# Optimization experiments

Hardware: AMD Instinct MI355X
Metric: run time of the kernel (lower is better)

## Reference

```python
import jax, jax.numpy as jnp
import numpy as np

LN_EPS = 1e-5  # torch LayerNorm default


def setup_inputs() -> dict:
    key = jax.random.key(0)
    ks = jax.random.split(key, 8)
    R, B, E, H, NREL = 100, 32, 15000, 16, 237
    return {
        "all_h": jax.random.randint(ks[0], (B,), 0, E, dtype=jnp.int64),
        "all_r": jnp.zeros((B,), dtype=jnp.int64),  # all queries share one relation (asserted in torch code)
        "rule_count": jax.random.randint(ks[1], (R, B, E), 0, 2, dtype=jnp.int32),  # grounding counts (sparse 0/1)
        "rule_emb": jax.random.normal(ks[2], (R, H), dtype=jnp.float32),
        "relation_emb": jax.random.normal(ks[3], (NREL, H), dtype=jnp.float32),
        "ln_g": jnp.ones((H,), dtype=jnp.float32),
        "ln_b": jnp.zeros((H,), dtype=jnp.float32),
        "W1": jax.random.normal(ks[4], (2 * H, 128), dtype=jnp.float32) * 0.1,
        "b1": jnp.zeros((128,), dtype=jnp.float32),
        "W2": jax.random.normal(ks[5], (128, 1), dtype=jnp.float32) * 0.1,
        "b2": jnp.zeros((1,), dtype=jnp.float32),
        "bias": jnp.zeros((E,), dtype=jnp.float32),
    }


def reference(all_h, all_r, rule_count, rule_emb, relation_emb, ln_g, ln_b, W1, b1, W2, b2, bias):
    # rule_count: [R, B, E] grounding counts; candidates are positions with any nonzero count.
    rc = rule_count.astype(jnp.float32)
    cand = rc.sum(0) > 0  # [B, E] candidate mask

    # FuncToNodeSum: weighted sum of rule embeddings per (batch, entity), then LayerNorm + ReLU.
    wvf = jnp.einsum('rbe,rh->beh', rc, rule_emb)  # [B, E, H]
    mu = wvf.mean(-1, keepdims=True)
    var = ((wvf - mu) ** 2).mean(-1, keepdims=True)
    vv = jax.nn.relu((wvf - mu) * jax.lax.rsqrt(var + LN_EPS) * ln_g + ln_b)

    # Concatenate query-relation embedding and score with MLP(2H -> 128 -> 1).
    rel = relation_emb[all_r[0]]  # [H]
    feat = jnp.concatenate([vv, jnp.broadcast_to(rel, vv.shape)], axis=-1)  # [B, E, 2H]
    h = jax.nn.relu(jnp.einsum('beh,hk->bek', feat, W1) + b1)
    out = (jnp.einsum('bek,ko->beo', h, W2) + b2)[..., 0]  # [B, E]

    # Scatter to candidates only (zeros elsewhere), then add entity bias (entity_feature='bias').
    score = jnp.where(cand, out, 0.0) + bias[None, :]
    return score
```

## Files before the change

kernel.cpp:

```cpp
#include <hip/hip_runtime.h>

#define NRULE 100
#define NB    32
#define NE    15000
#define NTOT  (NB * NE)
#define HD    16
#define KMID  128
#define LN_EPS 1e-5f

__global__ void precompute_c_kernel(const int* __restrict__ all_r,
                                    const float* __restrict__ relemb,
                                    const float* __restrict__ W1,
                                    const float* __restrict__ b1,
                                    float* __restrict__ cvec)
{
    const int k = threadIdx.x;
    if (k >= KMID) return;
    const int r = all_r[0];
    float t = b1[k];
#pragma unroll
    for (int h = 0; h < HD; ++h)
        t = fmaf(relemb[r * HD + h], W1[(HD + h) * KMID + k], t);
    cvec[k] = t;
}

__global__ __launch_bounds__(256) void predictor_main_kernel(
    const int*   __restrict__ rc,
    const float* __restrict__ remb,
    const float* __restrict__ ln_g,
    const float* __restrict__ ln_b,
    const float* __restrict__ W1,
    const float* __restrict__ W2,
    const float* __restrict__ b2,
    const float* __restrict__ bias,
    const float* __restrict__ cvec,
    float* __restrict__ out)
{
    const int tid  = blockIdx.x * blockDim.x + threadIdx.x;
    const int base = tid * 2;
    if (base >= NTOT) return;

    float acc0[HD], acc1[HD];
#pragma unroll
    for (int h = 0; h < HD; ++h) { acc0[h] = 0.f; acc1[h] = 0.f; }
    float ws0 = 0.f, ws1 = 0.f;

    const int* rcp = rc + base;
#pragma unroll 4
    for (int r = 0; r < NRULE; ++r) {
        const int2 p = *reinterpret_cast<const int2*>(rcp + r * NTOT);
        const float v0 = (float)p.x;
        const float v1 = (float)p.y;
        ws0 += v0; ws1 += v1;
#pragma unroll
        for (int h = 0; h < HD; ++h) {
            const float w = remb[r * HD + h];
            acc0[h] = fmaf(v0, w, acc0[h]);
            acc1[h] = fmaf(v1, w, acc1[h]);
        }
    }

    float vv0[HD], vv1[HD];
    {
        float mu0 = 0.f, mu1 = 0.f;
#pragma unroll
        for (int h = 0; h < HD; ++h) { mu0 += acc0[h]; mu1 += acc1[h]; }
        mu0 *= (1.f / HD); mu1 *= (1.f / HD);
        float var0 = 0.f, var1 = 0.f;
#pragma unroll
        for (int h = 0; h < HD; ++h) {
            const float d0 = acc0[h] - mu0;
            const float d1 = acc1[h] - mu1;
            var0 = fmaf(d0, d0, var0);
            var1 = fmaf(d1, d1, var1);
        }
        var0 *= (1.f / HD); var1 *= (1.f / HD);
        const float ri0 = rsqrtf(var0 + LN_EPS);
        const float ri1 = rsqrtf(var1 + LN_EPS);
#pragma unroll
        for (int h = 0; h < HD; ++h) {
            const float g = ln_g[h], bb = ln_b[h];
            vv0[h] = fmaxf(fmaf((acc0[h] - mu0) * ri0, g, bb), 0.f);
            vv1[h] = fmaxf(fmaf((acc1[h] - mu1) * ri1, g, bb), 0.f);
        }
    }

    const float b2v = b2[0];
    float o0 = b2v, o1 = b2v;
#pragma unroll 1
    for (int kc = 0; kc < KMID; kc += 16) {
        float t0[16], t1[16];
#pragma unroll
        for (int kk = 0; kk < 16; ++kk) {
            const float c = cvec[kc + kk];
            t0[kk] = c; t1[kk] = c;
        }
#pragma unroll
        for (int h = 0; h < HD; ++h) {
            const float a0 = vv0[h], a1 = vv1[h];
#pragma unroll
            for (int kk = 0; kk < 16; ++kk) {
                const float w = W1[h * KMID + kc + kk];
                t0[kk] = fmaf(a0, w, t0[kk]);
                t1[kk] = fmaf(a1, w, t1[kk]);
            }
        }
#pragma unroll
        for (int kk = 0; kk < 16; ++kk) {
            const float w2 = W2[kc + kk];
            o0 = fmaf(fmaxf(t0[kk], 0.f), w2, o0);
            o1 = fmaf(fmaxf(t1[kk], 0.f), w2, o1);
        }
    }

    o0 = (ws0 > 0.f) ? o0 : 0.f;
    o1 = (ws1 > 0.f) ? o1 : 0.f;
    const int m = base % NE;
    float2 res;
    res.x = o0 + bias[m];
    res.y = o1 + bias[m + 1];
    *reinterpret_cast<float2*>(out + base) = res;
}

extern "C" void kernel_launch(void* const* d_in, const int* in_sizes, int n_in,
                              void* d_out, int out_size, void* d_ws, size_t ws_size,
                              hipStream_t stream)
{
    const int*   all_r  = (const int*)d_in[1];
    const int*   rc     = (const int*)d_in[2];
    const float* remb   = (const float*)d_in[3];
    const float* relemb = (const float*)d_in[4];
    const float* ln_g   = (const float*)d_in[5];
    const float* ln_b   = (const float*)d_in[6];
    const float* W1     = (const float*)d_in[7];
    const float* b1     = (const float*)d_in[8];
    const float* W2     = (const float*)d_in[9];
    const float* b2     = (const float*)d_in[10];
    const float* bias   = (const float*)d_in[11];
    float* out  = (float*)d_out;
    float* cvec = (float*)d_ws;

    hipLaunchKernelGGL(precompute_c_kernel, dim3(1), dim3(128), 0, stream,
                       all_r, relemb, W1, b1, cvec);

    const int threads = NTOT / 2;
    const int blocks  = (threads + 255) / 256;
    hipLaunchKernelGGL(predictor_main_kernel, dim3(blocks), dim3(256), 0, stream,
                       rc, remb, ln_g, ln_b, W1, W2, b2, bias, cvec, out);
}
```

Before: 71.97 us.

## Use one element per thread with batched rule-count loads and higher occupancy

```diff
diff --git a/kernel.cpp b/kernel.cpp
--- a/kernel.cpp
+++ b/kernel.cpp
@@ -7,6 +7,7 @@
 #define HD    16
 #define KMID  128
 #define LN_EPS 1e-5f
+#define RCHUNK 20
 
 __global__ void precompute_c_kernel(const int* __restrict__ all_r,
                                     const float* __restrict__ relemb,
@@ -24,7 +25,7 @@
     cvec[k] = t;
 }
 
-__global__ __launch_bounds__(256) void predictor_main_kernel(
+__global__ __launch_bounds__(256, 8) void predictor_main_kernel(
     const int*   __restrict__ rc,
     const float* __restrict__ remb,
     const float* __restrict__ ln_g,
@@ -36,90 +37,69 @@
     const float* __restrict__ cvec,
     float* __restrict__ out)
 {
-    const int tid  = blockIdx.x * blockDim.x + threadIdx.x;
-    const int base = tid * 2;
-    if (base >= NTOT) return;
+    const int tid = blockIdx.x * blockDim.x + threadIdx.x;
+    if (tid >= NTOT) return;
 
-    float acc0[HD], acc1[HD];
+    float acc[HD];
 #pragma unroll
-    for (int h = 0; h < HD; ++h) { acc0[h] = 0.f; acc1[h] = 0.f; }
-    float ws0 = 0.f, ws1 = 0.f;
+    for (int h = 0; h < HD; ++h) acc[h] = 0.f;
+    float ws = 0.f;
 
-    const int* rcp = rc + base;
-#pragma unroll 4
-    for (int r = 0; r < NRULE; ++r) {
-        const int2 p = *reinterpret_cast<const int2*>(rcp + r * NTOT);
-        const float v0 = (float)p.x;
-        const float v1 = (float)p.y;
-        ws0 += v0; ws1 += v1;
+    const int* rcp = rc + tid;
 #pragma unroll
-        for (int h = 0; h < HD; ++h) {
-            const float w = remb[r * HD + h];
-            acc0[h] = fmaf(v0, w, acc0[h]);
-            acc1[h] = fmaf(v1, w, acc1[h]);
+    for (int r0 = 0; r0 < NRULE; r0 += RCHUNK) {
+        int v[RCHUNK];
+#pragma unroll
+        for (int i = 0; i < RCHUNK; ++i)
+            v[i] = rcp[(r0 + i) * NTOT];
+#pragma unroll
+        for (int i = 0; i < RCHUNK; ++i) {
+            const float f = (float)v[i];
+            ws += f;
+#pragma unroll
+            for (int h = 0; h < HD; ++h)
+                acc[h] = fmaf(f, remb[(r0 + i) * HD + h], acc[h]);
         }
     }
 
-    float vv0[HD], vv1[HD];
     {
-        float mu0 = 0.f, mu1 = 0.f;
+        float mu = 0.f;
 #pragma unroll
-        for (int h = 0; h < HD; ++h) { mu0 += acc0[h]; mu1 += acc1[h]; }
-        mu0 *= (1.f / HD); mu1 *= (1.f / HD);
-        float var0 = 0.f, var1 = 0.f;
+        for (int h = 0; h < HD; ++h) mu += acc[h];
+        mu *= (1.f / HD);
+        float var = 0.f;
 #pragma unroll
         for (int h = 0; h < HD; ++h) {
-            const float d0 = acc0[h] - mu0;
-            const float d1 = acc1[h] - mu1;
-            var0 = fmaf(d0, d0, var0);
-            var1 = fmaf(d1, d1, var1);
+            const float d = acc[h] - mu;
+            var = fmaf(d, d, var);
         }
-        var0 *= (1.f / HD); var1 *= (1.f / HD);
-        const float ri0 = rsqrtf(var0 + LN_EPS);
-        const float ri1 = rsqrtf(var1 + LN_EPS);
+        var *= (1.f / HD);
+        const float ri = rsqrtf(var + LN_EPS);
+#pragma unroll
+        for (int h = 0; h < HD; ++h)
+            acc[h] = fmaxf(fmaf((acc[h] - mu) * ri, ln_g[h], ln_b[h]), 0.f);
+    }
+
+    float o = b2[0];
+#pragma unroll 1
+    for (int kc = 0; kc < KMID; kc += 16) {
+        float t[16];
+#pragma unroll
+        for (int kk = 0; kk < 16; ++kk) t[kk] = cvec[kc + kk];
 #pragma unroll
         for (int h = 0; h < HD; ++h) {
-            const float g = ln_g[h], bb = ln_b[h];
-            vv0[h] = fmaxf(fmaf((acc0[h] - mu0) * ri0, g, bb), 0.f);
-            vv1[h] = fmaxf(fmaf((acc1[h] - mu1) * ri1, g, bb), 0.f);
+            const float a = acc[h];
+#pragma unroll
+            for (int kk = 0; kk < 16; ++kk)
+                t[kk] = fmaf(a, W1[h * KMID + kc + kk], t[kk]);
         }
+#pragma unroll
+        for (int kk = 0; kk < 16; ++kk)
+            o = fmaf(fmaxf(t[kk], 0.f), W2[kc + kk], o);
     }
 
-    const float b2v = b2[0];
-    float o0 = b2v, o1 = b2v;
-#pragma unroll 1
-    for (int kc = 0; kc < KMID; kc += 16) {
-        float t0[16], t1[16];
-#pragma unroll
-        for (int kk = 0; kk < 16; ++kk) {
-            const float c = cvec[kc + kk];
-            t0[kk] = c; t1[kk] = c;
-        }
-#pragma unroll
-        for (int h = 0; h < HD; ++h) {
-            const float a0 = vv0[h], a1 = vv1[h];
-#pragma unroll
-            for (int kk = 0; kk < 16; ++kk) {
-                const float w = W1[h * KMID + kc + kk];
-                t0[kk] = fmaf(a0, w, t0[kk]);
-                t1[kk] = fmaf(a1, w, t1[kk]);
-            }
-        }
-#pragma unroll
-        for (int kk = 0; kk < 16; ++kk) {
-            const float w2 = W2[kc + kk];
-            o0 = fmaf(fmaxf(t0[kk], 0.f), w2, o0);
-            o1 = fmaf(fmaxf(t1[kk], 0.f), w2, o1);
-        }
-    }
-
-    o0 = (ws0 > 0.f) ? o0 : 0.f;
-    o1 = (ws1 > 0.f) ? o1 : 0.f;
-    const int m = base % NE;
-    float2 res;
-    res.x = o0 + bias[m];
-    res.y = o1 + bias[m + 1];
-    *reinterpret_cast<float2*>(out + base) = res;
+    o = (ws > 0.f) ? o : 0.f;
+    out[tid] = o + bias[tid % NE];
 }
 
 extern "C" void kernel_launch(void* const* d_in, const int* in_sizes, int n_in,
@@ -143,8 +123,7 @@
     hipLaunchKernelGGL(precompute_c_kernel, dim3(1), dim3(128), 0, stream,
                        all_r, relemb, W1, b1, cvec);
 
-    const int threads = NTOT / 2;
-    const int blocks  = (threads + 255) / 256;
+    const int blocks = (NTOT + 255) / 256;
     hipLaunchKernelGGL(predictor_main_kernel, dim3(blocks), dim3(256), 0, stream,
                        rc, remb, ln_g, ln_b, W1, W2, b2, bias, cvec, out);
 }
```

Measured after the change: 132.2 us. +83.6%, slower.
